# Kernel optimization log

Hardware: AMD Instinct MI355X
Metric: run time of the kernel (lower is better)

The kernel has to match this reference:

```python
import jax, jax.numpy as jnp
import numpy as np

N_NODES = 50000
N_EDGES = 800000
IN_DIM, HID_DIM, OUT_DIM, N_HEADS = 256, 256, 64, 4
ATT_DIM = OUT_DIM * 2 + 1  # 129


def setup_inputs() -> dict:
    key = jax.random.key(0)
    ks = jax.random.split(key, 8)
    s = 0.05
    return {
        "x": jax.random.normal(ks[0], (N_NODES, IN_DIM), dtype=jnp.float32),
        "idx": jax.random.randint(ks[1], (2, N_EDGES), 0, N_NODES, dtype=jnp.int32),
        "elem": jax.random.uniform(ks[2], (N_EDGES,), dtype=jnp.float32),
        "W1": jax.random.normal(ks[3], (N_HEADS, IN_DIM, HID_DIM), dtype=jnp.float32) * s,
        "b1": jnp.zeros((N_HEADS, HID_DIM), jnp.float32),
        "W2": jax.random.normal(ks[4], (N_HEADS, HID_DIM, OUT_DIM), dtype=jnp.float32) * s,
        "b2": jnp.zeros((N_HEADS, OUT_DIM), jnp.float32),
        "A1": jax.random.normal(ks[5], (N_HEADS, ATT_DIM, ATT_DIM), dtype=jnp.float32) * s,
        "ab1": jnp.zeros((N_HEADS, ATT_DIM), jnp.float32),
        "A2": jax.random.normal(ks[6], (N_HEADS, ATT_DIM, 1), dtype=jnp.float32) * s,
        "ab2": jnp.zeros((N_HEADS, 1), jnp.float32),
    }


def reference(x, idx, elem, W1, b1, W2, b2, A1, ab1, A2, ab2):
    row, col = idx[0], idx[1]
    n = x.shape[0]

    def head(w1, bb1, w2, bb2, a1, aab1, a2, aab2):
        # 2-layer node MLP: [N, in] -> [N, out]
        feats = jnp.maximum(x @ w1 + bb1, 0.0) @ w2 + bb2
        # gather edge endpoints + edge value -> [E, 2*out+1]
        x_cat = jnp.concatenate([feats[row], feats[col], elem[:, None]], axis=1)
        # 2-layer edge attention MLP -> scalar per edge
        hid = jnp.maximum(x_cat @ a1 + aab1, 0.0)
        e1 = (hid @ a2 + aab2)[:, 0]
        e1 = jax.nn.leaky_relu(e1, negative_slope=0.2)
        w = jnp.exp(e1 - jnp.max(e1))  # global-max-stabilized exp
        # spmm: scatter weighted neighbor features into rows
        pooled = jax.ops.segment_sum(w[:, None] * feats[col], row, num_segments=n)
        row_sum = jax.ops.segment_sum(w, row, num_segments=n) + 1e-10
        return pooled / row_sum[:, None]  # [N, out]

    h = jax.vmap(head)(W1, b1, W2, b2, A1, ab1, A2, ab2)  # [H, N, out]
    return jnp.transpose(h, (1, 0, 2)).reshape(n, -1)  # concat heads -> [N, H*out]
```

## Files before the change

kernel.cpp:

```cpp
#include <hip/hip_runtime.h>
#include <hip/hip_bf16.h>

#define NNODES 50000
#define NEDGES 800000
#define IN_DIM 256
#define HID_DIM 256
#define OUT_DIM 64
#define NHEADS 4
#define ATT_DIM 129
#define PDIM 128
#define PJROWS 144
#define MAXD 64

#define XS_LD 264
#define FS_LD 72
#define PS_LD 144

#define LOG2E 1.44269504088896340736f

typedef unsigned short u16;
typedef unsigned char u8;
typedef unsigned int u32;
typedef __attribute__((ext_vector_type(8))) short bf16x8;
typedef __attribute__((ext_vector_type(4))) float f32x4;
typedef __attribute__((ext_vector_type(2))) float f32x2;
typedef __attribute__((ext_vector_type(2))) _Float16 h16x2;
typedef __fp16 hh2 __attribute__((ext_vector_type(2)));

__device__ __forceinline__ u16 f2bf(float f) {
  union { __hip_bfloat16 b; u16 u; } v;
  v.b = __float2bfloat16(f);
  return v.u;
}
__device__ __forceinline__ float bf2f(u16 b) {
  return __uint_as_float(((u32)b) << 16);
}
__device__ __forceinline__ h16x2 u2h2(u32 u) {
  union { u32 u; h16x2 h; } v; v.u = u; return v.h;
}
__device__ __forceinline__ u32 h2u(h16x2 h) {
  union { h16x2 h; u32 u; } v; v.h = h; return v.u;
}
__device__ __forceinline__ h16x2 pkrtz(float a, float b) {
  return __builtin_bit_cast(h16x2, __builtin_amdgcn_cvt_pkrtz(a, b));
}
__device__ __forceinline__ u32 cvt_pk_bf16(float a, float b) {
  u32 r;
  asm("v_cvt_pk_bf16_f32 %0, %1, %2" : "=v"(r) : "v"(a), "v"(b));
  return r;
}

__device__ __forceinline__ float dpp_sum16(float x) {
  int v;
  v = __builtin_amdgcn_update_dpp(0, __float_as_int(x), 0xB1, 0xF, 0xF, true);
  x += __int_as_float(v);
  v = __builtin_amdgcn_update_dpp(0, __float_as_int(x), 0x4E, 0xF, 0xF, true);
  x += __int_as_float(v);
  v = __builtin_amdgcn_update_dpp(0, __float_as_int(x), 0x141, 0xF, 0xF, true);
  x += __int_as_float(v);
  v = __builtin_amdgcn_update_dpp(0, __float_as_int(x), 0x140, 0xF, 0xF, true);
  x += __int_as_float(v);
  return x;
}

__global__ __launch_bounds__(256) void prep_kernel(
    const int* __restrict__ idx, const float* __restrict__ elem,
    const float* __restrict__ W1, const float* __restrict__ W2,
    const float* __restrict__ A1, const float* __restrict__ ab1,
    const float* __restrict__ A2, const float* __restrict__ ab2,
    u16* __restrict__ W1T, u16* __restrict__ W2T,
    u16* __restrict__ A1Tr, u16* __restrict__ A1Tc,
    uint4* __restrict__ thE, uint4* __restrict__ thA2, uint4* __restrict__ thB1,
    float4* __restrict__ th_tail, u32* __restrict__ cnt, u32* __restrict__ ce)
{
  int id = blockIdx.x * 256 + threadIdx.x;
  if (id < NEDGES) {
    int r = idx[id];
    u32 p = atomicAdd(&cnt[r], 1u);
    if (p < MAXD)
      ce[r * MAXD + p] = ((u32)f2bf(elem[id]) << 16) | (u32)idx[NEDGES + id];
  }
  if (id < NHEADS * 256 * 256) {
    int h = id >> 16, j = (id >> 8) & 255, k = id & 255;
    W1T[id] = f2bf(W1[(size_t)h * 65536 + k * 256 + j]);
  }
  if (id < NHEADS * 64 * 256) {
    int h = id >> 14, d = (id >> 8) & 63, j = id & 255;
    W2T[id] = f2bf(W2[(size_t)h * 16384 + j * 64 + d]);
  }
  if (id < NHEADS * PJROWS * 64) {
    int h = id / (PJROWS * 64);
    int rem = id % (PJROWS * 64);
    int j = rem >> 6, d = rem & 63;
    A1Tr[id] = (j < ATT_DIM) ? f2bf(A1[(size_t)h * 16641 + d * ATT_DIM + j]) : (u16)0;
    A1Tc[id] = (j < ATT_DIM) ? f2bf(A1[(size_t)h * 16641 + (64 + d) * ATT_DIM + j]) : (u16)0;
  }
  if (id < NHEADS * 16) {
    int h = id >> 4, m = id & 15;
    const float* Erow = A1 + (size_t)h * 16641 + (size_t)128 * ATT_DIM;
    uint4 e, a, b;
    u32* ep = (u32*)&e; u32* ap = (u32*)&a; u32* bp = (u32*)&b;
#pragma unroll
    for (int p = 0; p < 4; ++p) {
      int j = m * 8 + 2 * p;
      ep[p] = h2u(pkrtz(Erow[j], Erow[j + 1]));
      ap[p] = h2u(pkrtz(A2[h * ATT_DIM + j] * LOG2E, A2[h * ATT_DIM + j + 1] * LOG2E));
      bp[p] = h2u(pkrtz(ab1[h * ATT_DIM + j], ab1[h * ATT_DIM + j + 1]));
    }
    thE[id] = e; thA2[id] = a; thB1[id] = b;
  }
  if (id < NHEADS) {
    const float* Erow = A1 + (size_t)id * 16641 + (size_t)128 * ATT_DIM;
    th_tail[id] = make_float4(Erow[128], ab1[id * ATT_DIM + 128],
                              A2[id * ATT_DIM + 128] * LOG2E, ab2[id] * LOG2E);
  }
}

__global__ __launch_bounds__(256) void mlp_mfma_kernel(
    const float* __restrict__ x, const u16* __restrict__ W1T,
    const float* __restrict__ b1, const u16* __restrict__ W2T,
    const float* __restrict__ b2, const u16* __restrict__ A1Tr,
    const u16* __restrict__ A1Tc, u8* __restrict__ PF,
    u8* __restrict__ Pr8, u16* __restrict__ Prt, u16* __restrict__ Pct)
{
  __shared__ u16 xs[64 * XS_LD];
  __shared__ u16 hs[64 * XS_LD];
  __shared__ u16 fs[64 * FS_LD];
  u8* pc_s = (u8*)hs;
  u8* pr_s = (u8*)hs + 64 * PS_LD;
  const int n0 = blockIdx.x * 64;
  const int t = threadIdx.x;
  const int wv = t >> 6;
  const int l = t & 63;
  const int lr = l & 15;
  const int lq = l >> 4;

#pragma unroll
  for (int q = 0; q < 16; ++q) {
    int fi = q * 256 + t;
    int row = fi >> 6, c4 = fi & 63;
    int n = n0 + row;
    float4 v = make_float4(0.f, 0.f, 0.f, 0.f);
    if (n < NNODES) v = *(const float4*)(x + (size_t)n * IN_DIM + c4 * 4);
    ushort4 o;
    o.x = f2bf(v.x); o.y = f2bf(v.y); o.z = f2bf(v.z); o.w = f2bf(v.w);
    *(ushort4*)&xs[row * XS_LD + c4 * 4] = o;
  }
  __syncthreads();

  for (int hi = 0; hi < 2; ++hi) {
    const int h = (int)blockIdx.y + hi * 2;

    f32x4 acc[4][4];
#pragma unroll
    for (int ji = 0; ji < 4; ++ji)
#pragma unroll
      for (int ni = 0; ni < 4; ++ni) acc[ji][ni] = f32x4{0.f, 0.f, 0.f, 0.f};

    const u16* W1b = W1T + ((size_t)h * 256 + wv * 64) * 256;
#pragma unroll
    for (int kk = 0; kk < 8; ++kk) {
      const int ko = kk * 32 + lq * 8;
      bf16x8 w[4], xv[4];
#pragma unroll
      for (int ji = 0; ji < 4; ++ji)
        w[ji] = *(const bf16x8*)(W1b + (size_t)(ji * 16 + lr) * 256 + ko);
#pragma unroll
      for (int ni = 0; ni < 4; ++ni)
        xv[ni] = *(const bf16x8*)&xs[(ni * 16 + lr) * XS_LD + ko];
#pragma unroll
      for (int ji = 0; ji < 4; ++ji)
#pragma unroll
        for (int ni = 0; ni < 4; ++ni)
          acc[ji][ni] = __builtin_amdgcn_mfma_f32_16x16x32_bf16(w[ji], xv[ni], acc[ji][ni], 0, 0, 0);
    }
#pragma unroll
    for (int ji = 0; ji < 4; ++ji) {
      float4 bv = *(const float4*)(b1 + h * HID_DIM + wv * 64 + ji * 16 + lq * 4);
#pragma unroll
      for (int ni = 0; ni < 4; ++ni) {
        f32x4 v = acc[ji][ni];
        u32 lo = cvt_pk_bf16(fmaxf(v[0] + bv.x, 0.f), fmaxf(v[1] + bv.y, 0.f));
        u32 hi2 = cvt_pk_bf16(fmaxf(v[2] + bv.z, 0.f), fmaxf(v[3] + bv.w, 0.f));
        *(uint2*)&hs[(ni * 16 + lr) * XS_LD + wv * 64 + ji * 16 + lq * 4] = make_uint2(lo, hi2);
      }
    }
    __syncthreads();

    f32x4 acc2[4];
#pragma unroll
    for (int ni = 0; ni < 4; ++ni) acc2[ni] = f32x4{0.f, 0.f, 0.f, 0.f};
    const u16* W2b = W2T + ((size_t)h * 64 + wv * 16) * 256;
#pragma unroll
    for (int kk = 0; kk < 8; ++kk) {
      const int ko = kk * 32 + lq * 8;
      bf16x8 wd = *(const bf16x8*)(W2b + (size_t)lr * 256 + ko);
#pragma unroll
      for (int ni = 0; ni < 4; ++ni) {
        bf16x8 hv = *(const bf16x8*)&hs[(ni * 16 + lr) * XS_LD + ko];
        acc2[ni] = __builtin_amdgcn_mfma_f32_16x16x32_bf16(wd, hv, acc2[ni], 0, 0, 0);
      }
    }
    __syncthreads();
    {
      float4 bv = *(const float4*)(b2 + h * OUT_DIM + wv * 16 + lq * 4);
      const int d0 = wv * 16 + lq * 4;
#pragma unroll
      for (int ni = 0; ni < 4; ++ni) {
        f32x4 v = acc2[ni];
        u32 lo = cvt_pk_bf16(v[0] + bv.x, v[1] + bv.y);
        u32 hi2 = cvt_pk_bf16(v[2] + bv.z, v[3] + bv.w);
        *(uint2*)&fs[(ni * 16 + lr) * FS_LD + d0] = make_uint2(lo, hi2);
      }
    }
    __syncthreads();

    for (int c = wv; c < 18; c += 4) {
      const int rc = c / 9;
      const int nf = c % 9;
      const u16* Ab = (rc ? A1Tc : A1Tr) + ((size_t)h * PJROWS + nf * 16) * 64;
      f32x4 acc3[4];
#pragma unroll
      for (int ni = 0; ni < 4; ++ni) acc3[ni] = f32x4{0.f, 0.f, 0.f, 0.f};
#pragma unroll
      for (int kk = 0; kk < 2; ++kk) {
        const int ko = kk * 32 + lq * 8;
        bf16x8 aj = *(const bf16x8*)(Ab + (size_t)lr * 64 + ko);
#pragma unroll
        for (int ni = 0; ni < 4; ++ni) {
          bf16x8 fv = *(const bf16x8*)&fs[(ni * 16 + lr) * FS_LD + ko];
          acc3[ni] = __builtin_amdgcn_mfma_f32_16x16x32_bf16(aj, fv, acc3[ni], 0, 0, 0);
        }
      }
#pragma unroll
      for (int ni = 0; ni < 4; ++ni) {
        const int node = ni * 16 + lr;
        int n = n0 + node;
        if (n >= NNODES) continue;
        if (nf == 8) {
          if (lq == 0) {
            u16 vb = f2bf(acc3[ni][0]);
            if (rc == 0) Prt[(size_t)h * NNODES + n] = vb;
            else         Pct[(size_t)n * NHEADS + h] = vb;
          }
        } else {
          const int j0 = nf * 16 + lq * 4;
          f32x4 v = acc3[ni];
          u32 pk = __builtin_amdgcn_cvt_pk_fp8_f32(v[0], v[1], 0, false);
          pk = __builtin_amdgcn_cvt_pk_fp8_f32(v[2], v[3], pk, true);
          if (rc == 0) *(u32*)(pr_s + node * PS_LD + j0) = pk;
          else         *(u32*)(pc_s + node * PS_LD + j0) = pk;
        }
      }
    }
    __syncthreads();

#pragma unroll
    for (int it = 0; it < 4; ++it) {
      int flat = it * 256 + t;
      int node = flat >> 4, sub = flat & 15;
      int n = n0 + node;
      if (n < NNODES) {
        uint4 v;
        if (sub < 8) v = *(const uint4*)(pc_s + node * PS_LD + sub * 16);
        else         v = *(const uint4*)((const u8*)&fs[node * FS_LD] + (sub - 8) * 16);
        *(uint4*)(PF + (size_t)n * 1024 + h * 256 + sub * 16) = v;
      }
    }
#pragma unroll
    for (int it = 0; it < 2; ++it) {
      int flat = it * 256 + t;
      int node = flat >> 3, sub = flat & 7;
      int n = n0 + node;
      if (n < NNODES) {
        uint4 v = *(const uint4*)(pr_s + node * PS_LD + sub * 16);
        *(uint4*)(Pr8 + ((size_t)h * NNODES + n) * PDIM + sub * 16) = v;
      }
    }
    __syncthreads();
  }
}

__global__ __launch_bounds__(256) void edge_csr_kernel(
    const u8* __restrict__ PF, const u8* __restrict__ Pr8,
    const u16* __restrict__ Prt, const u16* __restrict__ Pct,
    const u32* __restrict__ cnt, const u32* __restrict__ ce,
    const uint4* __restrict__ thE, const uint4* __restrict__ thA2,
    const uint4* __restrict__ thB1, const float4* __restrict__ th_tail,
    float* __restrict__ out)
{
  const int r = blockIdx.x;
  const int h = threadIdx.x >> 6;
  const int l = threadIdx.x & 63;
  const int g = l >> 4;
  const int m = l & 15;

  const int deg = min((int)cnt[r], MAXD);
  if (deg == 0) {
    if (g == 0)
      *(float4*)(out + (size_t)r * (NHEADS * OUT_DIM) + h * OUT_DIM + m * 4) =
          make_float4(0.f, 0.f, 0.f, 0.f);
    return;
  }

  h16x2 Ej2[4], a2v2[4], prb2[4];
  {
    uint4 Eu = thE[h * 16 + m], Au = thA2[h * 16 + m], Bu = thB1[h * 16 + m];
    uint2 pr8v = *(const uint2*)(Pr8 + ((size_t)h * NNODES + r) * PDIM + m * 8);
    const u32* ep = (const u32*)&Eu;
    const u32* ap = (const u32*)&Au;
    const u32* bp = (const u32*)&Bu;
    f32x2 q01 = __builtin_amdgcn_cvt_pk_f32_fp8((int)pr8v.x, false);
    f32x2 q23 = __builtin_amdgcn_cvt_pk_f32_fp8((int)pr8v.x, true);
    f32x2 q45 = __builtin_amdgcn_cvt_pk_f32_fp8((int)pr8v.y, false);
    f32x2 q67 = __builtin_amdgcn_cvt_pk_f32_fp8((int)pr8v.y, true);
    h16x2 prh[4] = {pkrtz(q01[0], q01[1]), pkrtz(q23[0], q23[1]),
                    pkrtz(q45[0], q45[1]), pkrtz(q67[0], q67[1])};
#pragma unroll
    for (int p = 0; p < 4; ++p) {
      Ej2[p]  = u2h2(ep[p]);
      a2v2[p] = u2h2(ap[p]);
      prb2[p] = prh[p] + u2h2(bp[p]);
    }
  }
  const float4 tl = th_tail[h];
  float Et = 0.f, prtb = 0.f, a2t = 0.f;
  if (m == 0) {
    Et = tl.x;
    prtb = bf2f(Prt[(size_t)h * NNODES + r]) + tl.y;
    a2t = tl.z;
  }
  const float ab2v = tl.w;
  const h16x2 zero2 = {(_Float16)0.f, (_Float16)0.f};
  const u8* PFh = PF + h * 256;

  const u32* cebase = ce + r * MAXD;

  float acc0 = 0.f, acc1 = 0.f, acc2a = 0.f, acc3a = 0.f, wsum = 0.f;

  for (int k0 = 0; k0 < deg; k0 += 4) {
    const int e0 = k0 + g;
    u32 cv = cebase[(e0 < deg) ? e0 : (deg - 1)];
    u32 coloff = (cv & 0xffffu) << 10;
    float el = __uint_as_float(cv & 0xffff0000u);

    uint2 pc = *(const uint2*)(PFh + coloff + m * 8);
    ushort4 f4 = *(const ushort4*)(PFh + coloff + 128 + m * 8);
    float pctv = (m == 0) ? bf2f(Pct[(coloff >> 8) + h]) : 0.f;

    float tsum = fmaxf(fmaf(el, Et, prtb + pctv), 0.f) * a2t;

    f32x2 v01 = __builtin_amdgcn_cvt_pk_f32_fp8((int)pc.x, false);
    f32x2 v23 = __builtin_amdgcn_cvt_pk_f32_fp8((int)pc.x, true);
    f32x2 v45 = __builtin_amdgcn_cvt_pk_f32_fp8((int)pc.y, false);
    f32x2 v67 = __builtin_amdgcn_cvt_pk_f32_fp8((int)pc.y, true);
    h16x2 pch[4] = {pkrtz(v01[0], v01[1]), pkrtz(v23[0], v23[1]),
                    pkrtz(v45[0], v45[1]), pkrtz(v67[0], v67[1])};
    const h16x2 el2 = pkrtz(el, el);

#pragma unroll
    for (int p = 0; p < 4; ++p) {
      h16x2 s = prb2[p] + pch[p];
      s = __builtin_elementwise_fma(el2, Ej2[p], s);
      s = __builtin_elementwise_max(s, zero2);
      tsum = __builtin_amdgcn_fdot2(__builtin_bit_cast(hh2, s),
                                    __builtin_bit_cast(hh2, a2v2[p]), tsum, false);
    }

    tsum = dpp_sum16(tsum);

    float e1f = tsum + ab2v;
    e1f = fmaxf(e1f, 0.2f * e1f);
    float w = exp2f(e1f);
    w = (e0 < deg) ? w : 0.f;

    acc0  = fmaf(w, bf2f(f4.x), acc0);
    acc1  = fmaf(w, bf2f(f4.y), acc1);
    acc2a = fmaf(w, bf2f(f4.z), acc2a);
    acc3a = fmaf(w, bf2f(f4.w), acc3a);
    wsum += w;
  }

#pragma unroll
  for (int sh = 16; sh <= 32; sh <<= 1) {
    acc0  += __shfl_xor(acc0, sh);
    acc1  += __shfl_xor(acc1, sh);
    acc2a += __shfl_xor(acc2a, sh);
    acc3a += __shfl_xor(acc3a, sh);
    wsum  += __shfl_xor(wsum, sh);
  }
  if (g == 0) {
    float inv = 1.0f / (wsum + 1e-10f);
    float4 o = make_float4(acc0 * inv, acc1 * inv, acc2a * inv, acc3a * inv);
    *(float4*)(out + (size_t)r * (NHEADS * OUT_DIM) + h * OUT_DIM + m * 4) = o;
  }
}

extern "C" void kernel_launch(void* const* d_in, const int* in_sizes, int n_in,
                              void* d_out, int out_size, void* d_ws, size_t ws_size,
                              hipStream_t stream) {
  const float* x    = (const float*)d_in[0];
  const int*   idx  = (const int*)d_in[1];
  const float* elem = (const float*)d_in[2];
  const float* W1   = (const float*)d_in[3];
  const float* b1   = (const float*)d_in[4];
  const float* W2   = (const float*)d_in[5];
  const float* b2   = (const float*)d_in[6];
  const float* A1   = (const float*)d_in[7];
  const float* ab1  = (const float*)d_in[8];
  const float* A2   = (const float*)d_in[9];
  const float* ab2  = (const float*)d_in[10];
  float* out = (float*)d_out;

  u8*  Pr8 = (u8*)d_ws;
  u8*  PF  = Pr8 + (size_t)NHEADS * NNODES * PDIM;
  u16* Prt = (u16*)(PF + (size_t)NNODES * 1024);
  u16* Pct = Prt + (size_t)NHEADS * NNODES;
  u32* cnt = (u32*)(Pct + (size_t)NHEADS * NNODES);
  u32* ce  = cnt + NNODES;
  u16* W1T  = (u16*)(ce + (size_t)NNODES * MAXD);
  u16* W2T  = W1T + NHEADS * 256 * 256;
  u16* A1Tr = W2T + NHEADS * 64 * 256;
  u16* A1Tc = A1Tr + NHEADS * PJROWS * 64;
  uint4* thE  = (uint4*)(A1Tc + NHEADS * PJROWS * 64);
  uint4* thA2 = thE + NHEADS * 16;
  uint4* thB1 = thA2 + NHEADS * 16;
  float4* th_tail = (float4*)(thB1 + NHEADS * 16);

  (void)hipMemsetAsync(cnt, 0, (size_t)NNODES * sizeof(u32), stream);

  prep_kernel<<<(NEDGES + 255) / 256, 256, 0, stream>>>(
      idx, elem, W1, W2, A1, ab1, A2, ab2, W1T, W2T, A1Tr, A1Tc,
      thE, thA2, thB1, th_tail, cnt, ce);

  dim3 gridM((NNODES + 63) / 64, 2);
  mlp_mfma_kernel<<<gridM, 256, 0, stream>>>(x, W1T, b1, W2T, b2, A1Tr, A1Tc,
                                             PF, Pr8, Prt, Pct);

  edge_csr_kernel<<<NNODES, 256, 0, stream>>>(PF, Pr8, Prt, Pct, cnt, ce,
                                              thE, thA2, thB1, th_tail, out);
}
```

Before: 337.8 us.

## Halve MLP node tile to 32 and widen edge lanes to 8 features

The node MLP kernel now processes 32 nodes per block instead of 64, which doubles the grid and shrinks shared memory use, to improve occupancy and load balance. The edge kernel now has each lane handle 8 features instead of 4, so 8 edges run in parallel per wave instead of 4. This gives wider vector loads, a shorter DPP reduction and half the loop trips for typical degrees. The trade-off is that W1/W2 weights are reloaded for every smaller tile, and more per-edge padding is wasted when the degree is not a multiple of 8.

Result: slower. 351.7 us (+4.1%).

```diff
diff --git a/kernel.cpp b/kernel.cpp
--- a/kernel.cpp
+++ b/kernel.cpp
@@ -12,6 +12,7 @@
 #define PJROWS 144
 #define MAXD 64
 
+#define NPB 32
 #define XS_LD 264
 #define FS_LD 72
 #define PS_LD 144
@@ -50,15 +51,13 @@
   return r;
 }
 
-__device__ __forceinline__ float dpp_sum16(float x) {
+__device__ __forceinline__ float dpp_sum8(float x) {
   int v;
   v = __builtin_amdgcn_update_dpp(0, __float_as_int(x), 0xB1, 0xF, 0xF, true);
   x += __int_as_float(v);
   v = __builtin_amdgcn_update_dpp(0, __float_as_int(x), 0x4E, 0xF, 0xF, true);
   x += __int_as_float(v);
   v = __builtin_amdgcn_update_dpp(0, __float_as_int(x), 0x141, 0xF, 0xF, true);
-  x += __int_as_float(v);
-  v = __builtin_amdgcn_update_dpp(0, __float_as_int(x), 0x140, 0xF, 0xF, true);
   x += __int_as_float(v);
   return x;
 }
@@ -123,12 +122,12 @@
     const u16* __restrict__ A1Tc, u8* __restrict__ PF,
     u8* __restrict__ Pr8, u16* __restrict__ Prt, u16* __restrict__ Pct)
 {
-  __shared__ u16 xs[64 * XS_LD];
-  __shared__ u16 hs[64 * XS_LD];
-  __shared__ u16 fs[64 * FS_LD];
+  __shared__ u16 xs[NPB * XS_LD];
+  __shared__ u16 hs[NPB * XS_LD];
+  __shared__ u16 fs[NPB * FS_LD];
   u8* pc_s = (u8*)hs;
-  u8* pr_s = (u8*)hs + 64 * PS_LD;
-  const int n0 = blockIdx.x * 64;
+  u8* pr_s = (u8*)hs + NPB * PS_LD;
+  const int n0 = blockIdx.x * NPB;
   const int t = threadIdx.x;
   const int wv = t >> 6;
   const int l = t & 63;
@@ -136,7 +135,7 @@
   const int lq = l >> 4;
 
 #pragma unroll
-  for (int q = 0; q < 16; ++q) {
+  for (int q = 0; q < 8; ++q) {
     int fi = q * 256 + t;
     int row = fi >> 6, c4 = fi & 63;
     int n = n0 + row;
@@ -151,34 +150,34 @@
   for (int hi = 0; hi < 2; ++hi) {
     const int h = (int)blockIdx.y + hi * 2;
 
-    f32x4 acc[4][4];
+    f32x4 acc[4][2];
 #pragma unroll
     for (int ji = 0; ji < 4; ++ji)
 #pragma unroll
-      for (int ni = 0; ni < 4; ++ni) acc[ji][ni] = f32x4{0.f, 0.f, 0.f, 0.f};
+      for (int ni = 0; ni < 2; ++ni) acc[ji][ni] = f32x4{0.f, 0.f, 0.f, 0.f};
 
     const u16* W1b = W1T + ((size_t)h * 256 + wv * 64) * 256;
 #pragma unroll
     for (int kk = 0; kk < 8; ++kk) {
       const int ko = kk * 32 + lq * 8;
-      bf16x8 w[4], xv[4];
+      bf16x8 w[4], xv[2];
 #pragma unroll
       for (int ji = 0; ji < 4; ++ji)
         w[ji] = *(const bf16x8*)(W1b + (size_t)(ji * 16 + lr) * 256 + ko);
 #pragma unroll
-      for (int ni = 0; ni < 4; ++ni)
+      for (int ni = 0; ni < 2; ++ni)
         xv[ni] = *(const bf16x8*)&xs[(ni * 16 + lr) * XS_LD + ko];
 #pragma unroll
       for (int ji = 0; ji < 4; ++ji)
 #pragma unroll
-        for (int ni = 0; ni < 4; ++ni)
+        for (int ni = 0; ni < 2; ++ni)
           acc[ji][ni] = __builtin_amdgcn_mfma_f32_16x16x32_bf16(w[ji], xv[ni], acc[ji][ni], 0, 0, 0);
     }
 #pragma unroll
     for (int ji = 0; ji < 4; ++ji) {
       float4 bv = *(const float4*)(b1 + h * HID_DIM + wv * 64 + ji * 16 + lq * 4);
 #pragma unroll
-      for (int ni = 0; ni < 4; ++ni) {
+      for (int ni = 0; ni < 2; ++ni) {
         f32x4 v = acc[ji][ni];
         u32 lo = cvt_pk_bf16(fmaxf(v[0] + bv.x, 0.f), fmaxf(v[1] + bv.y, 0.f));
         u32 hi2 = cvt_pk_bf16(fmaxf(v[2] + bv.z, 0.f), fmaxf(v[3] + bv.w, 0.f));
@@ -187,16 +186,16 @@
     }
     __syncthreads();
 
-    f32x4 acc2[4];
-#pragma unroll
-    for (int ni = 0; ni < 4; ++ni) acc2[ni] = f32x4{0.f, 0.f, 0.f, 0.f};
+    f32x4 acc2[2];
+#pragma unroll
+    for (int ni = 0; ni < 2; ++ni) acc2[ni] = f32x4{0.f, 0.f, 0.f, 0.f};
     const u16* W2b = W2T + ((size_t)h * 64 + wv * 16) * 256;
 #pragma unroll
     for (int kk = 0; kk < 8; ++kk) {
       const int ko = kk * 32 + lq * 8;
       bf16x8 wd = *(const bf16x8*)(W2b + (size_t)lr * 256 + ko);
 #pragma unroll
-      for (int ni = 0; ni < 4; ++ni) {
+      for (int ni = 0; ni < 2; ++ni) {
         bf16x8 hv = *(const bf16x8*)&hs[(ni * 16 + lr) * XS_LD + ko];
         acc2[ni] = __builtin_amdgcn_mfma_f32_16x16x32_bf16(wd, hv, acc2[ni], 0, 0, 0);
       }
@@ -206,7 +205,7 @@
       float4 bv = *(const float4*)(b2 + h * OUT_DIM + wv * 16 + lq * 4);
       const int d0 = wv * 16 + lq * 4;
 #pragma unroll
-      for (int ni = 0; ni < 4; ++ni) {
+      for (int ni = 0; ni < 2; ++ni) {
         f32x4 v = acc2[ni];
         u32 lo = cvt_pk_bf16(v[0] + bv.x, v[1] + bv.y);
         u32 hi2 = cvt_pk_bf16(v[2] + bv.z, v[3] + bv.w);
@@ -219,21 +218,21 @@
       const int rc = c / 9;
       const int nf = c % 9;
       const u16* Ab = (rc ? A1Tc : A1Tr) + ((size_t)h * PJROWS + nf * 16) * 64;
-      f32x4 acc3[4];
-#pragma unroll
-      for (int ni = 0; ni < 4; ++ni) acc3[ni] = f32x4{0.f, 0.f, 0.f, 0.f};
+      f32x4 acc3[2];
+#pragma unroll
+      for (int ni = 0; ni < 2; ++ni) acc3[ni] = f32x4{0.f, 0.f, 0.f, 0.f};
 #pragma unroll
       for (int kk = 0; kk < 2; ++kk) {
         const int ko = kk * 32 + lq * 8;
         bf16x8 aj = *(const bf16x8*)(Ab + (size_t)lr * 64 + ko);
 #pragma unroll
-        for (int ni = 0; ni < 4; ++ni) {
+        for (int ni = 0; ni < 2; ++ni) {
           bf16x8 fv = *(const bf16x8*)&fs[(ni * 16 + lr) * FS_LD + ko];
           acc3[ni] = __builtin_amdgcn_mfma_f32_16x16x32_bf16(aj, fv, acc3[ni], 0, 0, 0);
         }
       }
 #pragma unroll
-      for (int ni = 0; ni < 4; ++ni) {
+      for (int ni = 0; ni < 2; ++ni) {
         const int node = ni * 16 + lr;
         int n = n0 + node;
         if (n >= NNODES) continue;
@@ -256,7 +255,7 @@
     __syncthreads();
 
 #pragma unroll
-    for (int it = 0; it < 4; ++it) {
+    for (int it = 0; it < 2; ++it) {
       int flat = it * 256 + t;
       int node = flat >> 4, sub = flat & 15;
       int n = n0 + node;
@@ -267,10 +266,8 @@
         *(uint4*)(PF + (size_t)n * 1024 + h * 256 + sub * 16) = v;
       }
     }
-#pragma unroll
-    for (int it = 0; it < 2; ++it) {
-      int flat = it * 256 + t;
-      int node = flat >> 3, sub = flat & 7;
+    {
+      int node = t >> 3, sub = t & 7;
       int n = n0 + node;
       if (n < NNODES) {
         uint4 v = *(const uint4*)(pr_s + node * PS_LD + sub * 16);
@@ -292,35 +289,44 @@
   const int r = blockIdx.x;
   const int h = threadIdx.x >> 6;
   const int l = threadIdx.x & 63;
-  const int g = l >> 4;
-  const int m = l & 15;
+  const int g = l >> 3;
+  const int m = l & 7;
 
   const int deg = min((int)cnt[r], MAXD);
   if (deg == 0) {
-    if (g == 0)
-      *(float4*)(out + (size_t)r * (NHEADS * OUT_DIM) + h * OUT_DIM + m * 4) =
-          make_float4(0.f, 0.f, 0.f, 0.f);
+    if (g == 0) {
+      float4 z = make_float4(0.f, 0.f, 0.f, 0.f);
+      float* o = out + (size_t)r * (NHEADS * OUT_DIM) + h * OUT_DIM + m * 8;
+      *(float4*)o = z; *(float4*)(o + 4) = z;
+    }
     return;
   }
 
-  h16x2 Ej2[4], a2v2[4], prb2[4];
+  h16x2 Ej2[8], a2v2[8], prb2[8];
   {
-    uint4 Eu = thE[h * 16 + m], Au = thA2[h * 16 + m], Bu = thB1[h * 16 + m];
-    uint2 pr8v = *(const uint2*)(Pr8 + ((size_t)h * NNODES + r) * PDIM + m * 8);
-    const u32* ep = (const u32*)&Eu;
-    const u32* ap = (const u32*)&Au;
-    const u32* bp = (const u32*)&Bu;
-    f32x2 q01 = __builtin_amdgcn_cvt_pk_f32_fp8((int)pr8v.x, false);
-    f32x2 q23 = __builtin_amdgcn_cvt_pk_f32_fp8((int)pr8v.x, true);
-    f32x2 q45 = __builtin_amdgcn_cvt_pk_f32_fp8((int)pr8v.y, false);
-    f32x2 q67 = __builtin_amdgcn_cvt_pk_f32_fp8((int)pr8v.y, true);
-    h16x2 prh[4] = {pkrtz(q01[0], q01[1]), pkrtz(q23[0], q23[1]),
-                    pkrtz(q45[0], q45[1]), pkrtz(q67[0], q67[1])};
-#pragma unroll
-    for (int p = 0; p < 4; ++p) {
-      Ej2[p]  = u2h2(ep[p]);
-      a2v2[p] = u2h2(ap[p]);
-      prb2[p] = prh[p] + u2h2(bp[p]);
+    uint4 pr8v = *(const uint4*)(Pr8 + ((size_t)h * NNODES + r) * PDIM + m * 16);
+    const u32* pw = (const u32*)&pr8v;
+#pragma unroll
+    for (int half = 0; half < 2; ++half) {
+      uint4 Eu = thE[h * 16 + 2 * m + half];
+      uint4 Au = thA2[h * 16 + 2 * m + half];
+      uint4 Bu = thB1[h * 16 + 2 * m + half];
+      const u32* ep = (const u32*)&Eu;
+      const u32* ap = (const u32*)&Au;
+      const u32* bp = (const u32*)&Bu;
+#pragma unroll
+      for (int p = 0; p < 2; ++p) {
+        u32 w8 = pw[half * 2 + p];
+        f32x2 qa = __builtin_amdgcn_cvt_pk_f32_fp8((int)w8, false);
+        f32x2 qb = __builtin_amdgcn_cvt_pk_f32_fp8((int)w8, true);
+        int o = half * 4 + p * 2;
+        Ej2[o]      = u2h2(ep[p * 2]);
+        Ej2[o + 1]  = u2h2(ep[p * 2 + 1]);
+        a2v2[o]     = u2h2(ap[p * 2]);
+        a2v2[o + 1] = u2h2(ap[p * 2 + 1]);
+        prb2[o]     = pkrtz(qa[0], qa[1]) + u2h2(bp[p * 2]);
+        prb2[o + 1] = pkrtz(qb[0], qb[1]) + u2h2(bp[p * 2 + 1]);
+      }
     }
   }
   const float4 tl = th_tail[h];
@@ -336,63 +342,68 @@
 
   const u32* cebase = ce + r * MAXD;
 
-  float acc0 = 0.f, acc1 = 0.f, acc2a = 0.f, acc3a = 0.f, wsum = 0.f;
-
-  for (int k0 = 0; k0 < deg; k0 += 4) {
+  float acc[8];
+#pragma unroll
+  for (int q = 0; q < 8; ++q) acc[q] = 0.f;
+  float wsum = 0.f;
+
+  for (int k0 = 0; k0 < deg; k0 += 8) {
     const int e0 = k0 + g;
     u32 cv = cebase[(e0 < deg) ? e0 : (deg - 1)];
     u32 coloff = (cv & 0xffffu) << 10;
     float el = __uint_as_float(cv & 0xffff0000u);
 
-    uint2 pc = *(const uint2*)(PFh + coloff + m * 8);
-    ushort4 f4 = *(const ushort4*)(PFh + coloff + 128 + m * 8);
+    uint4 pc = *(const uint4*)(PFh + coloff + m * 16);
+    uint4 f4 = *(const uint4*)(PFh + coloff + 128 + m * 16);
     float pctv = (m == 0) ? bf2f(Pct[(coloff >> 8) + h]) : 0.f;
 
     float tsum = fmaxf(fmaf(el, Et, prtb + pctv), 0.f) * a2t;
 
-    f32x2 v01 = __builtin_amdgcn_cvt_pk_f32_fp8((int)pc.x, false);
-    f32x2 v23 = __builtin_amdgcn_cvt_pk_f32_fp8((int)pc.x, true);
-    f32x2 v45 = __builtin_amdgcn_cvt_pk_f32_fp8((int)pc.y, false);
-    f32x2 v67 = __builtin_amdgcn_cvt_pk_f32_fp8((int)pc.y, true);
-    h16x2 pch[4] = {pkrtz(v01[0], v01[1]), pkrtz(v23[0], v23[1]),
-                    pkrtz(v45[0], v45[1]), pkrtz(v67[0], v67[1])};
+    const u32* pcw = (const u32*)&pc;
     const h16x2 el2 = pkrtz(el, el);
-
 #pragma unroll
     for (int p = 0; p < 4; ++p) {
-      h16x2 s = prb2[p] + pch[p];
-      s = __builtin_elementwise_fma(el2, Ej2[p], s);
-      s = __builtin_elementwise_max(s, zero2);
-      tsum = __builtin_amdgcn_fdot2(__builtin_bit_cast(hh2, s),
-                                    __builtin_bit_cast(hh2, a2v2[p]), tsum, false);
-    }
-
-    tsum = dpp_sum16(tsum);
+      f32x2 va = __builtin_amdgcn_cvt_pk_f32_fp8((int)pcw[p], false);
+      f32x2 vb = __builtin_amdgcn_cvt_pk_f32_fp8((int)pcw[p], true);
+      h16x2 s0 = prb2[p * 2] + pkrtz(va[0], va[1]);
+      h16x2 s1 = prb2[p * 2 + 1] + pkrtz(vb[0], vb[1]);
+      s0 = __builtin_elementwise_fma(el2, Ej2[p * 2], s0);
+      s1 = __builtin_elementwise_fma(el2, Ej2[p * 2 + 1], s1);
+      s0 = __builtin_elementwise_max(s0, zero2);
+      s1 = __builtin_elementwise_max(s1, zero2);
+      tsum = __builtin_amdgcn_fdot2(__builtin_bit_cast(hh2, s0),
+                                    __builtin_bit_cast(hh2, a2v2[p * 2]), tsum, false);
+      tsum = __builtin_amdgcn_fdot2(__builtin_bit_cast(hh2, s1),
+                                    __builtin_bit_cast(hh2, a2v2[p * 2 + 1]), tsum, false);
+    }
+
+    tsum = dpp_sum8(tsum);
 
     float e1f = tsum + ab2v;
     e1f = fmaxf(e1f, 0.2f * e1f);
     float w = exp2f(e1f);
     w = (e0 < deg) ? w : 0.f;
 
-    acc0  = fmaf(w, bf2f(f4.x), acc0);
-    acc1  = fmaf(w, bf2f(f4.y), acc1);
-    acc2a = fmaf(w, bf2f(f4.z), acc2a);
-    acc3a = fmaf(w, bf2f(f4.w), acc3a);
+    const u32* fw = (const u32*)&f4;
+#pragma unroll
+    for (int p = 0; p < 4; ++p) {
+      acc[p * 2]     = fmaf(w, __uint_as_float(fw[p] << 16), acc[p * 2]);
+      acc[p * 2 + 1] = fmaf(w, __uint_as_float(fw[p] & 0xffff0000u), acc[p * 2 + 1]);
+    }
     wsum += w;
   }
 
 #pragma unroll
-  for (int sh = 16; sh <= 32; sh <<= 1) {
-    acc0  += __shfl_xor(acc0, sh);
-    acc1  += __shfl_xor(acc1, sh);
-    acc2a += __shfl_xor(acc2a, sh);
-    acc3a += __shfl_xor(acc3a, sh);
-    wsum  += __shfl_xor(wsum, sh);
+  for (int sh = 8; sh <= 32; sh <<= 1) {
+#pragma unroll
+    for (int q = 0; q < 8; ++q) acc[q] += __shfl_xor(acc[q], sh);
+    wsum += __shfl_xor(wsum, sh);
   }
   if (g == 0) {
     float inv = 1.0f / (wsum + 1e-10f);
-    float4 o = make_float4(acc0 * inv, acc1 * inv, acc2a * inv, acc3a * inv);
-    *(float4*)(out + (size_t)r * (NHEADS * OUT_DIM) + h * OUT_DIM + m * 4) = o;
+    float* o = out + (size_t)r * (NHEADS * OUT_DIM) + h * OUT_DIM + m * 8;
+    *(float4*)o = make_float4(acc[0] * inv, acc[1] * inv, acc[2] * inv, acc[3] * inv);
+    *(float4*)(o + 4) = make_float4(acc[4] * inv, acc[5] * inv, acc[6] * inv, acc[7] * inv);
   }
 }
 
@@ -433,7 +444,7 @@
       idx, elem, W1, W2, A1, ab1, A2, ab2, W1T, W2T, A1Tr, A1Tc,
       thE, thA2, thB1, th_tail, cnt, ce);
 
-  dim3 gridM((NNODES + 63) / 64, 2);
+  dim3 gridM((NNODES + NPB - 1) / NPB, 2);
   mlp_mfma_kernel<<<gridM, 256, 0, stream>>>(x, W1T, b1, W2T, b2, A1Tr, A1Tc,
                                              PF, Pr8, Prt, Pct);
 
```
